# Performance work log

Hardware: AMD Instinct MI355X
Metric: run time of the kernel (lower is better)

## Reference

```python
import jax, jax.numpy as jnp
import numpy as np
from jax import lax

# fixed finite-difference kernels (HWIO)
KXN = jnp.asarray([[0., -1., 1.]], dtype=jnp.float32).reshape(1, 3, 1, 1)
KXP = jnp.asarray([[-1., 1., 0.]], dtype=jnp.float32).reshape(1, 3, 1, 1)
KYN = jnp.asarray([[1.], [-1.], [0.]], dtype=jnp.float32).reshape(3, 1, 1, 1)
KYP = jnp.asarray([[0.], [1.], [-1.]], dtype=jnp.float32).reshape(3, 1, 1, 1)


def conv2d(x, k):
    # NHWC input, HWIO kernel, SAME padding, stride 1
    return lax.conv_general_dilated(x, k, (1, 1), 'SAME',
                                    dimension_numbers=('NHWC', 'HWIO', 'NHWC'))


def setup_inputs() -> dict:
    key = jax.random.key(0)
    ks = jax.random.split(key, 11)
    B, H, W = 8, 512, 512
    return {
        'u': jax.random.normal(ks[0], (B, H, W, 1), jnp.float32),
        'image': jax.random.uniform(ks[1], (B, H, W, 1), jnp.float32),
        'conv_kernel_x': jax.random.normal(ks[2], (3, 3, 1, 32), jnp.float32) * 0.05,
        'conv_kernel_y': jax.random.normal(ks[3], (3, 3, 1, 32), jnp.float32) * 0.05,
        'sep_kernel_depthwise': jax.random.normal(ks[4], (3, 3, 1, 8), jnp.float32) * 0.05,
        'sep_kernel_pointwise': jax.random.normal(ks[5], (1, 1, 8, 8), jnp.float32) * 0.05,
        'conv_kernel_curve_0': jax.random.normal(ks[6], (5, 5, 1, 8), jnp.float32) * 0.05,
        'conv_kernel_curve_1': jax.random.normal(ks[7], (5, 5, 8, 8), jnp.float32) * 0.05,
        'conv_kernel_curve_2': jax.random.normal(ks[8], (3, 3, 8, 16), jnp.float32) * 0.05,
        'conv_kernel_smoother': jax.random.normal(ks[9], (5, 5, 1, 1), jnp.float32) * 0.05,
        'kappa_kernel': jax.random.normal(ks[10], (H, W, 1), jnp.float32) * 0.05,
    }


def reference(u, image, conv_kernel_x, conv_kernel_y, sep_kernel_depthwise,
              sep_kernel_pointwise, conv_kernel_curve_0, conv_kernel_curve_1,
              conv_kernel_curve_2, conv_kernel_smoother, kappa_kernel):
    # separable conv on the (fixed) image: in_ch=1 so depthwise == standard conv
    edges = conv2d(conv2d(image, sep_kernel_depthwise), sep_kernel_pointwise)
    edges = jnp.sum(jax.nn.relu(edges), axis=-1, keepdims=True)
    edges = jax.nn.soft_sign(edges)  # x / (1 + |x|)

    grad_edges_x = jnp.sum(jax.nn.relu(conv2d(edges, conv_kernel_x)), axis=-1, keepdims=True)
    grad_edges_y = jnp.sum(jax.nn.relu(conv2d(edges, conv_kernel_y)), axis=-1, keepdims=True)

    xp = conv2d(u, KXP)
    xn = conv2d(u, KXN)
    yp = conv2d(u, KYP)
    yn = conv2d(u, KYN)

    fxp = jax.nn.relu(grad_edges_x)
    fxn = -jax.nn.relu(-grad_edges_x)
    fyp = jax.nn.relu(grad_edges_y)
    fyn = -jax.nn.relu(-grad_edges_y)

    kappa = conv2d(conv2d(conv2d(u, conv_kernel_curve_0), conv_kernel_curve_1), conv_kernel_curve_2)
    kappa = jnp.sum(kappa, axis=-1, keepdims=True)
    kappa = kappa * kappa_kernel  # (H,W,1) broadcasts over batch
    kappa = conv2d(kappa, conv_kernel_smoother)

    return u + fxp * xp + fxn * xn + fyp * yp + fyn * yn + edges + kappa
```

## Files before the change

### kernel.cpp

```cpp
#include <hip/hip_runtime.h>
#include <cstddef>

#define HH 512
#define WW 512
#define BB 8
#define T  32

#define F0    256
#define KT0   1280
#define E0    4096
#define MAPW  520
#define MAPB  (512 * MAPW)
#define K0    (E0 + BB * MAPB)
#define WS_NEEDED_BYTES ((size_t)(K0 + BB * MAPB) * 4)

typedef __attribute__((ext_vector_type(8))) short short8;
typedef __attribute__((ext_vector_type(4))) float float4v;

__device__ inline unsigned short f2bf(float f) {
  unsigned u = __builtin_bit_cast(unsigned, f);
  unsigned r = (u + 0x7FFFu + ((u >> 16) & 1u)) >> 16;
  return (unsigned short)r;
}

__global__ __launch_bounds__(256) void precompute_kernels(
    const float* __restrict__ kd,
    const float* __restrict__ kp,
    const float* __restrict__ k0,
    const float* __restrict__ k1,
    const float* __restrict__ k2,
    const float* __restrict__ kx,
    const float* __restrict__ ky,
    float* __restrict__ ws) {
  __shared__ float k9[648];
  __shared__ float k2s[72];
  __shared__ float kef[121];
  const int tid = threadIdx.x;

  for (int idx = tid; idx < 72; idx += 256) {
    int c = idx & 7, pq = idx >> 3;
    float s = 0.f;
    for (int c0 = 0; c0 < 8; ++c0) s = fmaf(kd[pq * 8 + c0], kp[c0 * 8 + c], s);
    ws[idx] = s;
  }
  for (int idx = tid; idx < 72; idx += 256) {
    int c1 = idx & 7, tv = idx >> 3;
    float s = 0.f;
    for (int c2 = 0; c2 < 16; ++c2) s += k2[(tv * 8 + c1) * 16 + c2];
    k2s[idx] = s;
  }
  for (int idx = tid; idx < 648; idx += 256) {
    int c1 = idx & 7;
    int ab = idx >> 3;
    int a = ab / 9, b = ab % 9;
    float s = 0.f;
    int plo = a > 4 ? a - 4 : 0, phi = a < 4 ? a : 4;
    int qlo = b > 4 ? b - 4 : 0, qhi = b < 4 ? b : 4;
    for (int p = plo; p <= phi; ++p)
      for (int q = qlo; q <= qhi; ++q) {
        int r = a - p, sx = b - q;
        const float* k0p = &k0[(p * 5 + q) * 8];
        const float* k1p = &k1[((r * 5 + sx) * 8) * 8 + c1];
        for (int c0 = 0; c0 < 8; ++c0) s = fmaf(k0p[c0], k1p[c0 * 8], s);
      }
    k9[idx] = s;
  }
  for (int idx = tid; idx < 2048; idx += 256) {
    int nt = idx >> 9, ln = (idx >> 3) & 63, j = idx & 7;
    int k = (ln >> 4) * 8 + j;
    int n = nt * 16 + (ln & 15);
    float v = 0.f;
    if (k < 9) v = (n < 32) ? kx[k * 32 + n] : ky[k * 32 + (n - 32)];
    ((unsigned short*)ws)[F0 * 2 + idx] = f2bf(v);
  }
  __syncthreads();
  for (int idx = tid; idx < 121; idx += 256) {
    int A = idx / 11, B = idx % 11;
    float s = 0.f;
    int tlo = A > 8 ? A - 8 : 0, thi = A < 2 ? A : 2;
    int vlo = B > 8 ? B - 8 : 0, vhi = B < 2 ? B : 2;
    for (int t = tlo; t <= thi; ++t)
      for (int v = vlo; v <= vhi; ++v) {
        int a = A - t, b = B - v;
        for (int c1 = 0; c1 < 8; ++c1)
          s = fmaf(k9[(a * 9 + b) * 8 + c1], k2s[(t * 3 + v) * 8 + c1], s);
      }
    ws[72 + idx] = s;
    kef[idx] = s;
  }
  __syncthreads();
  for (int idx = tid; idx < 5632; idx += 256) {
    int b = idx >> 9, ln = (idx >> 3) & 63, j = idx & 7;
    int m = ln & 15;
    int k = (ln >> 4) * 8 + j;
    int a = k - m - 3;
    float v = ((unsigned)a < 11u) ? kef[a * 11 + b] : 0.f;
    ((unsigned short*)ws)[KT0 * 2 + idx] = f2bf(v);
  }
}

__global__ __launch_bounds__(256) void kernelA(
    const float* __restrict__ u, const float* __restrict__ img,
    const float* __restrict__ kk, const float* ws,
    float* maps) {
  __shared__ unsigned short suT[42 * 56];
  __shared__ float si[34 * 36];

  const int bx = blockIdx.x * T, by = blockIdx.y * T, b = blockIdx.z;
  const int tid = threadIdx.x;
  const float* ub = u + (size_t)b * HH * WW;
  const float* ib = img + (size_t)b * HH * WW;

  for (int idx = tid; idx < 48 * 42; idx += 256) {
    int r = idx / 42, c = idx % 42;
    int gy = by - 8 + r, gx = bx - 5 + c;
    float v = 0.f;
    if ((unsigned)gy < HH && (unsigned)gx < WW) v = ub[gy * WW + gx];
    suT[c * 56 + r] = f2bf(v);
  }
  for (int idx = tid; idx < 34 * 34; idx += 256) {
    int i = idx / 34, j = idx % 34;
    int gy = by - 1 + i, gx = bx - 1 + j;
    float v = 0.f;
    if ((unsigned)gy < HH && (unsigned)gx < WW) v = ib[gy * WW + gx];
    si[i * 36 + j] = v;
  }
  __syncthreads();

  {
    const int oy = tid >> 3, ox = (tid & 7) * 4;
    const int gy = by + oy, gx = bx + ox;

    float acc[8][4];
    #pragma unroll
    for (int c = 0; c < 8; ++c)
      #pragma unroll
      for (int t = 0; t < 4; ++t) acc[c][t] = 0.f;
    #pragma unroll
    for (int p = 0; p < 3; ++p) {
      const float* srow = &si[(oy + p) * 36 + ox];
      float4 r4 = *reinterpret_cast<const float4*>(srow);
      float2 r2 = *reinterpret_cast<const float2*>(srow + 4);
      float r[6] = {r4.x, r4.y, r4.z, r4.w, r2.x, r2.y};
      #pragma unroll
      for (int q = 0; q < 3; ++q) {
        float4 w0 = *reinterpret_cast<const float4*>(&ws[(p * 3 + q) * 8]);
        float4 w1 = *reinterpret_cast<const float4*>(&ws[(p * 3 + q) * 8 + 4]);
        #pragma unroll
        for (int t = 0; t < 4; ++t) {
          float v = r[q + t];
          acc[0][t] = fmaf(v, w0.x, acc[0][t]);
          acc[1][t] = fmaf(v, w0.y, acc[1][t]);
          acc[2][t] = fmaf(v, w0.z, acc[2][t]);
          acc[3][t] = fmaf(v, w0.w, acc[3][t]);
          acc[4][t] = fmaf(v, w1.x, acc[4][t]);
          acc[5][t] = fmaf(v, w1.y, acc[5][t]);
          acc[6][t] = fmaf(v, w1.z, acc[6][t]);
          acc[7][t] = fmaf(v, w1.w, acc[7][t]);
        }
      }
    }
    float ev[4];
    #pragma unroll
    for (int t = 0; t < 4; ++t) {
      float e = 0.f;
      #pragma unroll
      for (int c = 0; c < 8; ++c) e += fmaxf(acc[c][t], 0.f);
      ev[t] = e / (1.f + e);
    }
    float* erow = maps + E0 + (size_t)b * MAPB + (size_t)gy * MAPW + 4 + gx;
    *reinterpret_cast<float4*>(erow) = make_float4(ev[0], ev[1], ev[2], ev[3]);

    if (bx == 0 && (tid & 7) == 0) {
      float4 z = make_float4(0.f, 0.f, 0.f, 0.f);
      *reinterpret_cast<float4*>(maps + E0 + (size_t)b * MAPB + (size_t)gy * MAPW) = z;
      *reinterpret_cast<float4*>(maps + K0 + (size_t)b * MAPB + (size_t)gy * MAPW) = z;
    }
    if (bx == WW - T && (tid & 7) == 7) {
      float4 z = make_float4(0.f, 0.f, 0.f, 0.f);
      *reinterpret_cast<float4*>(maps + E0 + (size_t)b * MAPB + (size_t)gy * MAPW + 516) = z;
      *reinterpret_cast<float4*>(maps + K0 + (size_t)b * MAPB + (size_t)gy * MAPW + 516) = z;
    }
  }

  {
    const int lane = tid & 63;
    const int wv   = tid >> 6;
    const int q    = lane >> 4;
    const int n    = lane & 15;
    const int sty  = wv >> 1, stx = wv & 1;

    const unsigned short* KT = ((const unsigned short*)ws) + KT0 * 2;

    float4v acc = {0.f, 0.f, 0.f, 0.f};
    #pragma unroll
    for (int bb = 0; bb < 11; ++bb) {
      short8 af = *reinterpret_cast<const short8*>(KT + (bb * 64 + lane) * 8);
      short8 bf = *reinterpret_cast<const short8*>(
          &suT[(stx * 16 + n + bb) * 56 + sty * 16 + q * 8]);
      acc = __builtin_amdgcn_mfma_f32_16x16x32_bf16(af, bf, acc, 0, 0, 0);
    }
    float* kmapb = maps + K0 + (size_t)b * MAPB;
    #pragma unroll
    for (int i = 0; i < 4; ++i) {
      int yy = by + sty * 16 + q * 4 + i;
      int xx = bx + stx * 16 + n;
      kmapb[(size_t)yy * MAPW + 4 + xx] = acc[i] * kk[(size_t)yy * WW + xx];
    }
  }
}

__global__ __launch_bounds__(256) void kernelB(
    const float* __restrict__ u,
    const float* __restrict__ sm,
    const float* maps, float* __restrict__ out) {
  __shared__ float sgx[32 * 32];
  __shared__ float sgy[32 * 32];

  const int bx = blockIdx.x * T, by = blockIdx.y * T, b = blockIdx.z;
  const int tid = threadIdx.x;
  const float* emap = maps + E0 + (size_t)b * MAPB;
  const float* kmap = maps + K0 + (size_t)b * MAPB;
  const float* ub   = u + (size_t)b * HH * WW;

  const int lane = tid & 63;
  const int wv   = tid >> 6;
  const int q    = lane >> 4;
  const int m    = lane & 15;

  short8 afr[4];
  {
    const unsigned short* F = ((const unsigned short*)maps) + F0 * 2;
    #pragma unroll
    for (int t = 0; t < 4; ++t)
      afr[t] = *reinterpret_cast<const short8*>(F + (t * 64 + lane) * 8);
  }

  const int gy0 = by + wv * 8;

  #pragma unroll
  for (int h = 0; h < 32; h += 16) {
    const int gxl = bx + h + m;
    const float* colp = emap + 4 + gxl - 1;

    unsigned short W[9];
    #pragma unroll
    for (int d = 0; d < 3; ++d) {
      int ry = gy0 - 1 + d;
      int rc = ry < 0 ? 0 : (ry > HH - 1 ? HH - 1 : ry);
      float msk = (ry == rc) ? 1.f : 0.f;
      const float* rp = colp + (size_t)rc * MAPW;
      W[3 * d + 0] = f2bf(rp[0] * msk);
      W[3 * d + 1] = f2bf(rp[1] * msk);
      W[3 * d + 2] = f2bf(rp[2] * msk);
    }

    #pragma unroll
    for (int r = 0; r < 8; ++r) {
      short8 bv = (short8)0;
      if (q == 0) {
        #pragma unroll
        for (int j = 0; j < 8; ++j) bv[j] = (short)W[j];
      } else if (q == 1) {
        bv[0] = (short)W[8];
      }

      float4v c0 = {0.f, 0.f, 0.f, 0.f}, c1 = c0, c2 = c0, c3 = c0;
      c0 = __builtin_amdgcn_mfma_f32_16x16x32_bf16(afr[0], bv, c0, 0, 0, 0);
      c1 = __builtin_amdgcn_mfma_f32_16x16x32_bf16(afr[1], bv, c1, 0, 0, 0);
      c2 = __builtin_amdgcn_mfma_f32_16x16x32_bf16(afr[2], bv, c2, 0, 0, 0);
      c3 = __builtin_amdgcn_mfma_f32_16x16x32_bf16(afr[3], bv, c3, 0, 0, 0);

      float rx = 0.f, ry = 0.f;
      #pragma unroll
      for (int i = 0; i < 4; ++i) {
        rx += fmaxf(c0[i], 0.f) + fmaxf(c1[i], 0.f);
        ry += fmaxf(c2[i], 0.f) + fmaxf(c3[i], 0.f);
      }
      rx += __shfl_xor(rx, 16); rx += __shfl_xor(rx, 32);
      ry += __shfl_xor(ry, 16); ry += __shfl_xor(ry, 32);

      if (q == 0) {
        sgx[(wv * 8 + r) * 32 + h + m] = rx;
        sgy[(wv * 8 + r) * 32 + h + m] = ry;
      }

      if (r < 7) {
        #pragma unroll
        for (int t = 0; t < 6; ++t) W[t] = W[t + 3];
        int ryn = gy0 + r + 2;
        int rcn = ryn < 0 ? 0 : (ryn > HH - 1 ? HH - 1 : ryn);
        float msk = (ryn == rcn) ? 1.f : 0.f;
        const float* rp = colp + (size_t)rcn * MAPW;
        W[6] = f2bf(rp[0] * msk);
        W[7] = f2bf(rp[1] * msk);
        W[8] = f2bf(rp[2] * msk);
      }
    }
  }
  __syncthreads();

  {
    const int oy = tid >> 3, ox = (tid & 7) * 4;
    const int gy = by + oy, gx = bx + ox;

    float4 gx4 = *reinterpret_cast<const float4*>(&sgx[oy * 32 + ox]);
    float4 gy4 = *reinterpret_cast<const float4*>(&sgy[oy * 32 + ox]);
    float gxa[4] = {gx4.x, gx4.y, gx4.z, gx4.w};
    float gya[4] = {gy4.x, gy4.y, gy4.z, gy4.w};

    float4 ec4 = *reinterpret_cast<const float4*>(&emap[(size_t)gy * MAPW + 4 + gx]);
    float ec[4] = {ec4.x, ec4.y, ec4.z, ec4.w};

    float kap[4] = {0.f, 0.f, 0.f, 0.f};
    #pragma unroll
    for (int m5 = 0; m5 < 5; ++m5) {
      int ry = gy - 2 + m5;
      int rc = ry < 0 ? 0 : (ry > HH - 1 ? HH - 1 : ry);
      float msk = (ry == rc) ? 1.f : 0.f;
      const float* row = kmap + (size_t)rc * MAPW + 4 + gx;
      float2 a  = *reinterpret_cast<const float2*>(row - 2);
      float4 c4 = *reinterpret_cast<const float4*>(row);
      float2 d2 = *reinterpret_cast<const float2*>(row + 4);
      float r[8] = {a.x, a.y, c4.x, c4.y, c4.z, c4.w, d2.x, d2.y};
      #pragma unroll
      for (int n = 0; n < 5; ++n) {
        float w = sm[m5 * 5 + n] * msk;
        #pragma unroll
        for (int t = 0; t < 4; ++t) kap[t] = fmaf(r[t + n], w, kap[t]);
      }
    }

    const float* ur = ub + (size_t)gy * WW + gx;
    float4 uc4 = *reinterpret_cast<const float4*>(ur);
    int jm = gx > 0 ? -1 : 0;
    float ul = ur[jm];
    ul = gx > 0 ? ul : 0.f;
    int ryd = gy < HH - 1 ? gy + 1 : HH - 1;
    float md = gy < HH - 1 ? 1.f : 0.f;
    float4 ud4 = *reinterpret_cast<const float4*>(ub + (size_t)ryd * WW + gx);

    float uc[4]  = {uc4.x, uc4.y, uc4.z, uc4.w};
    float ulx[4] = {ul, uc4.x, uc4.y, uc4.z};
    float udn[4] = {ud4.x * md, ud4.y * md, ud4.z * md, ud4.w * md};

    float res[4];
    #pragma unroll
    for (int t = 0; t < 4; ++t) {
      float xp = uc[t] - ulx[t];
      float yp = uc[t] - udn[t];
      res[t] = uc[t] + gxa[t] * xp + gya[t] * yp + ec[t] + kap[t];
    }
    *reinterpret_cast<float4*>(&out[((size_t)b * HH + gy) * WW + gx]) =
        make_float4(res[0], res[1], res[2], res[3]);
  }
}

__global__ __launch_bounds__(256) void forcing_main(
    const float* __restrict__ u, const float* __restrict__ img,
    const float* __restrict__ kx, const float* __restrict__ ky,
    const float* __restrict__ sm, const float* __restrict__ kk,
    const float* __restrict__ ws, float* __restrict__ out) {
  __shared__ float su[46][48];
  __shared__ float si[36][37];
  __shared__ float se[34][35];
  __shared__ float sk[36][37];
  __shared__ float w_edge[72];
  __shared__ float w_kx[288];
  __shared__ float w_ky[288];
  __shared__ float w_k11[124];
  __shared__ float w_sm[28];

  const int bx = blockIdx.x * T;
  const int by = blockIdx.y * T;
  const int b  = blockIdx.z;
  const int tid = threadIdx.x;
  const float* ub = u   + (size_t)b * HH * WW;
  const float* ib = img + (size_t)b * HH * WW;

  for (int i = tid; i < 72; i += 256)  w_edge[i] = ws[i];
  for (int i = tid; i < 121; i += 256) w_k11[i]  = ws[72 + i];
  for (int i = tid; i < 288; i += 256) { w_kx[i] = kx[i]; w_ky[i] = ky[i]; }
  if (tid < 25) w_sm[tid] = sm[tid];

  for (int idx = tid; idx < 46 * 46; idx += 256) {
    int i = idx / 46, j = idx % 46;
    int gy = by - 7 + i, gx = bx - 7 + j;
    float v = 0.f;
    if ((unsigned)gy < HH && (unsigned)gx < WW) v = ub[gy * WW + gx];
    su[i][j] = v;
  }
  for (int idx = tid; idx < 36 * 36; idx += 256) {
    int i = idx / 36, j = idx % 36;
    int gy = by - 2 + i, gx = bx - 2 + j;
    float v = 0.f;
    if ((unsigned)gy < HH && (unsigned)gx < WW) v = ib[gy * WW + gx];
    si[i][j] = v;
  }
  __syncthreads();

  for (int idx = tid; idx < 34 * 9; idx += 256) {
    int i = idx / 9, j0 = (idx % 9) * 4;
    float acc[8][4];
    #pragma unroll
    for (int c = 0; c < 8; ++c)
      #pragma unroll
      for (int t = 0; t < 4; ++t) acc[c][t] = 0.f;
    #pragma unroll
    for (int p = 0; p < 3; ++p) {
      float r[6];
      #pragma unroll
      for (int t = 0; t < 6; ++t) r[t] = si[i + p][j0 + t];
      #pragma unroll
      for (int q = 0; q < 3; ++q) {
        const float4 w0 = *reinterpret_cast<const float4*>(&w_edge[(p * 3 + q) * 8]);
        const float4 w1 = *reinterpret_cast<const float4*>(&w_edge[(p * 3 + q) * 8 + 4]);
        #pragma unroll
        for (int t = 0; t < 4; ++t) {
          float v = r[q + t];
          acc[0][t] = fmaf(v, w0.x, acc[0][t]);
          acc[1][t] = fmaf(v, w0.y, acc[1][t]);
          acc[2][t] = fmaf(v, w0.z, acc[2][t]);
          acc[3][t] = fmaf(v, w0.w, acc[3][t]);
          acc[4][t] = fmaf(v, w1.x, acc[4][t]);
          acc[5][t] = fmaf(v, w1.y, acc[5][t]);
          acc[6][t] = fmaf(v, w1.z, acc[6][t]);
          acc[7][t] = fmaf(v, w1.w, acc[7][t]);
        }
      }
    }
    int gy = by - 1 + i;
    #pragma unroll
    for (int t = 0; t < 4; ++t) {
      int j = j0 + t;
      if (j < 34) {
        int gx = bx - 1 + j;
        float val = 0.f;
        if ((unsigned)gy < HH && (unsigned)gx < WW) {
          float e = 0.f;
          #pragma unroll
          for (int c = 0; c < 8; ++c) e += fmaxf(acc[c][t], 0.f);
          val = e / (1.f + e);
        }
        se[i][j] = val;
      }
    }
  }

  for (int idx = tid; idx < 36 * 9; idx += 256) {
    int i = idx / 9, js = (idx % 9) * 4;
    float o0 = 0.f, o1 = 0.f, o2 = 0.f, o3 = 0.f;
    #pragma unroll
    for (int A = 0; A < 11; ++A) {
      const float* row = &su[i + A][js];
      float4 v0 = *reinterpret_cast<const float4*>(row);
      float4 v1 = *reinterpret_cast<const float4*>(row + 4);
      float4 v2 = *reinterpret_cast<const float4*>(row + 8);
      float r[14] = {v0.x, v0.y, v0.z, v0.w, v1.x, v1.y, v1.z, v1.w,
                     v2.x, v2.y, v2.z, v2.w, row[12], row[13]};
      #pragma unroll
      for (int B2 = 0; B2 < 11; ++B2) {
        float w = w_k11[A * 11 + B2];
        o0 = fmaf(r[B2],     w, o0);
        o1 = fmaf(r[B2 + 1], w, o1);
        o2 = fmaf(r[B2 + 2], w, o2);
        o3 = fmaf(r[B2 + 3], w, o3);
      }
    }
    int gy = by - 2 + i;
    float o[4] = {o0, o1, o2, o3};
    #pragma unroll
    for (int t = 0; t < 4; ++t) {
      int gx = bx - 2 + js + t;
      float val = 0.f;
      if ((unsigned)gy < HH && (unsigned)gx < WW) val = o[t] * kk[gy * WW + gx];
      sk[i][js + t] = val;
    }
  }
  __syncthreads();

  {
    const int oy = tid >> 3;
    const int ox = (tid & 7) * 4;
    const int gy = by + oy;
    const int gx = bx + ox;

    float e[3][6];
    #pragma unroll
    for (int p = 0; p < 3; ++p)
      #pragma unroll
      for (int t = 0; t < 6; ++t) e[p][t] = se[oy + p][ox + t];

    const float4* wx4 = reinterpret_cast<const float4*>(w_kx);
    const float4* wy4 = reinterpret_cast<const float4*>(w_ky);

    float gxa[4] = {0.f, 0.f, 0.f, 0.f};
    float gya[4] = {0.f, 0.f, 0.f, 0.f};
    #pragma unroll
    for (int cq = 0; cq < 8; ++cq) {
      float sx[4][4], sy[4][4];
      #pragma unroll
      for (int cc = 0; cc < 4; ++cc)
        #pragma unroll
        for (int t = 0; t < 4; ++t) { sx[cc][t] = 0.f; sy[cc][t] = 0.f; }
      #pragma unroll
      for (int p = 0; p < 3; ++p)
        #pragma unroll
        for (int q = 0; q < 3; ++q) {
          float4 wx = wx4[(p * 3 + q) * 8 + cq];
          float4 wy = wy4[(p * 3 + q) * 8 + cq];
          #pragma unroll
          for (int t = 0; t < 4; ++t) {
            float evv = e[p][q + t];
            sx[0][t] = fmaf(evv, wx.x, sx[0][t]);
            sx[1][t] = fmaf(evv, wx.y, sx[1][t]);
            sx[2][t] = fmaf(evv, wx.z, sx[2][t]);
            sx[3][t] = fmaf(evv, wx.w, sx[3][t]);
            sy[0][t] = fmaf(evv, wy.x, sy[0][t]);
            sy[1][t] = fmaf(evv, wy.y, sy[1][t]);
            sy[2][t] = fmaf(evv, wy.z, sy[2][t]);
            sy[3][t] = fmaf(evv, wy.w, sy[3][t]);
          }
        }
      #pragma unroll
      for (int cc = 0; cc < 4; ++cc)
        #pragma unroll
        for (int t = 0; t < 4; ++t) {
          gxa[t] += fmaxf(sx[cc][t], 0.f);
          gya[t] += fmaxf(sy[cc][t], 0.f);
        }
    }

    float res[4];
    #pragma unroll
    for (int t = 0; t < 4; ++t) {
      float kap = 0.f;
      #pragma unroll
      for (int m = 0; m < 5; ++m)
        #pragma unroll
        for (int n = 0; n < 5; ++n)
          kap = fmaf(sk[oy + m][ox + t + n], w_sm[m * 5 + n], kap);

      float uc = su[oy + 7][ox + 7 + t];
      float xp = uc - su[oy + 7][ox + 6 + t];
      float yp = uc - su[oy + 8][ox + 7 + t];
      float ec = se[oy + 1][ox + 1 + t];
      res[t] = uc + gxa[t] * xp + gya[t] * yp + ec + kap;
    }

    float4 r4 = make_float4(res[0], res[1], res[2], res[3]);
    *reinterpret_cast<float4*>(&out[((size_t)b * HH + gy) * WW + gx]) = r4;
  }
}

extern "C" void kernel_launch(void* const* d_in, const int* in_sizes, int n_in,
                              void* d_out, int out_size, void* d_ws, size_t ws_size,
                              hipStream_t stream) {
  const float* u   = (const float*)d_in[0];
  const float* img = (const float*)d_in[1];
  const float* kx  = (const float*)d_in[2];
  const float* ky  = (const float*)d_in[3];
  const float* kd  = (const float*)d_in[4];
  const float* kp  = (const float*)d_in[5];
  const float* k0  = (const float*)d_in[6];
  const float* k1  = (const float*)d_in[7];
  const float* k2  = (const float*)d_in[8];
  const float* sm  = (const float*)d_in[9];
  const float* kk  = (const float*)d_in[10];
  float* out = (float*)d_out;
  float* ws  = (float*)d_ws;

  precompute_kernels<<<1, 256, 0, stream>>>(kd, kp, k0, k1, k2, kx, ky, ws);
  dim3 grid(WW / T, HH / T, BB);
  if (ws != nullptr && ws_size >= WS_NEEDED_BYTES) {
    kernelA<<<grid, 256, 0, stream>>>(u, img, kk, ws, ws);
    kernelB<<<grid, 256, 0, stream>>>(u, sm, ws, out);
  } else {
    forcing_main<<<grid, 256, 0, stream>>>(u, img, kx, ky, sm, kk, ws, out);
  }
}
```

Before: 143.8 us.

## Fuse edge/kappa map kernel and gradient/output kernel into one halo-recompute kernel

Merges the two-pass pipeline (kernelA writing edge and kappa maps to global workspace, kernelB reading them back) into a single kernel that keeps those intermediate maps in shared memory. Each tile now computes edges and kappa over an enlarged halo (34x34 and 36x36) so the neighbouring 3x3 and 5x5 stencils can be applied locally. This removes the global write/read of two 8x512x520 float maps and one kernel launch. In exchange it adds redundant halo computation, more MFMA tiles (9 instead of 4) and much larger LDS use, which may lower occupancy.

```diff
diff --git a/kernel.cpp b/kernel.cpp
--- a/kernel.cpp
+++ b/kernel.cpp
@@ -8,11 +8,7 @@
 
 #define F0    256
 #define KT0   1280
-#define E0    4096
-#define MAPW  520
-#define MAPB  (512 * MAPW)
-#define K0    (E0 + BB * MAPB)
-#define WS_NEEDED_BYTES ((size_t)(K0 + BB * MAPB) * 4)
+#define WS_NEEDED_BYTES ((size_t)4096 * 4)
 
 typedef __attribute__((ext_vector_type(8))) short short8;
 typedef __attribute__((ext_vector_type(4))) float float4v;
@@ -99,38 +95,46 @@
   }
 }
 
-__global__ __launch_bounds__(256) void kernelA(
+__global__ __launch_bounds__(256) void fused(
     const float* __restrict__ u, const float* __restrict__ img,
-    const float* __restrict__ kk, const float* ws,
-    float* maps) {
-  __shared__ unsigned short suT[42 * 56];
-  __shared__ float si[34 * 36];
+    const float* __restrict__ kk, const float* __restrict__ sm,
+    const float* __restrict__ ws, float* __restrict__ out) {
+  __shared__ unsigned short suT[58 * 72];
+  __shared__ float si[36 * 36];
+  __shared__ float se32[34 * 35];
+  __shared__ unsigned short sebf[34 * 36];
+  __shared__ float skp[36 * 37];
+  __shared__ float sgx[32 * 32];
+  __shared__ float sgy[32 * 32];
 
   const int bx = blockIdx.x * T, by = blockIdx.y * T, b = blockIdx.z;
   const int tid = threadIdx.x;
   const float* ub = u + (size_t)b * HH * WW;
   const float* ib = img + (size_t)b * HH * WW;
 
-  for (int idx = tid; idx < 48 * 42; idx += 256) {
-    int r = idx / 42, c = idx % 42;
-    int gy = by - 8 + r, gx = bx - 5 + c;
+  const int lane = tid & 63;
+  const int wv   = tid >> 6;
+  const int q    = lane >> 4;
+  const int m    = lane & 15;
+
+  for (int idx = tid; idx < 64 * 58; idx += 256) {
+    int r = idx / 58, c = idx % 58;
+    int gy = by - 10 + r, gx = bx - 7 + c;
     float v = 0.f;
     if ((unsigned)gy < HH && (unsigned)gx < WW) v = ub[gy * WW + gx];
-    suT[c * 56 + r] = f2bf(v);
-  }
-  for (int idx = tid; idx < 34 * 34; idx += 256) {
-    int i = idx / 34, j = idx % 34;
-    int gy = by - 1 + i, gx = bx - 1 + j;
+    suT[c * 72 + r] = f2bf(v);
+  }
+  for (int idx = tid; idx < 36 * 36; idx += 256) {
+    int i = idx / 36, j = idx % 36;
+    int gy = by - 2 + i, gx = bx - 2 + j;
     float v = 0.f;
     if ((unsigned)gy < HH && (unsigned)gx < WW) v = ib[gy * WW + gx];
     si[i * 36 + j] = v;
   }
   __syncthreads();
 
-  {
-    const int oy = tid >> 3, ox = (tid & 7) * 4;
-    const int gy = by + oy, gx = bx + ox;
-
+  for (int idx = tid; idx < 34 * 9; idx += 256) {
+    int i = idx / 9, j0 = (idx % 9) * 4;
     float acc[8][4];
     #pragma unroll
     for (int c = 0; c < 8; ++c)
@@ -138,17 +142,16 @@
       for (int t = 0; t < 4; ++t) acc[c][t] = 0.f;
     #pragma unroll
     for (int p = 0; p < 3; ++p) {
-      const float* srow = &si[(oy + p) * 36 + ox];
-      float4 r4 = *reinterpret_cast<const float4*>(srow);
-      float2 r2 = *reinterpret_cast<const float2*>(srow + 4);
-      float r[6] = {r4.x, r4.y, r4.z, r4.w, r2.x, r2.y};
-      #pragma unroll
-      for (int q = 0; q < 3; ++q) {
-        float4 w0 = *reinterpret_cast<const float4*>(&ws[(p * 3 + q) * 8]);
-        float4 w1 = *reinterpret_cast<const float4*>(&ws[(p * 3 + q) * 8 + 4]);
+      float r[6];
+      #pragma unroll
+      for (int t = 0; t < 6; ++t) r[t] = si[(i + p) * 36 + j0 + t];
+      #pragma unroll
+      for (int qq = 0; qq < 3; ++qq) {
+        float4 w0 = *reinterpret_cast<const float4*>(&ws[(p * 3 + qq) * 8]);
+        float4 w1 = *reinterpret_cast<const float4*>(&ws[(p * 3 + qq) * 8 + 4]);
         #pragma unroll
         for (int t = 0; t < 4; ++t) {
-          float v = r[q + t];
+          float v = r[qq + t];
           acc[0][t] = fmaf(v, w0.x, acc[0][t]);
           acc[1][t] = fmaf(v, w0.y, acc[1][t]);
           acc[2][t] = fmaf(v, w0.z, acc[2][t]);
@@ -160,141 +163,105 @@
         }
       }
     }
-    float ev[4];
+    int gy = by - 1 + i;
     #pragma unroll
     for (int t = 0; t < 4; ++t) {
-      float e = 0.f;
-      #pragma unroll
-      for (int c = 0; c < 8; ++c) e += fmaxf(acc[c][t], 0.f);
-      ev[t] = e / (1.f + e);
-    }
-    float* erow = maps + E0 + (size_t)b * MAPB + (size_t)gy * MAPW + 4 + gx;
-    *reinterpret_cast<float4*>(erow) = make_float4(ev[0], ev[1], ev[2], ev[3]);
-
-    if (bx == 0 && (tid & 7) == 0) {
-      float4 z = make_float4(0.f, 0.f, 0.f, 0.f);
-      *reinterpret_cast<float4*>(maps + E0 + (size_t)b * MAPB + (size_t)gy * MAPW) = z;
-      *reinterpret_cast<float4*>(maps + K0 + (size_t)b * MAPB + (size_t)gy * MAPW) = z;
-    }
-    if (bx == WW - T && (tid & 7) == 7) {
-      float4 z = make_float4(0.f, 0.f, 0.f, 0.f);
-      *reinterpret_cast<float4*>(maps + E0 + (size_t)b * MAPB + (size_t)gy * MAPW + 516) = z;
-      *reinterpret_cast<float4*>(maps + K0 + (size_t)b * MAPB + (size_t)gy * MAPW + 516) = z;
+      int j = j0 + t;
+      if (j < 34) {
+        int gx = bx - 1 + j;
+        float val = 0.f;
+        if ((unsigned)gy < HH && (unsigned)gx < WW) {
+          float e = 0.f;
+          #pragma unroll
+          for (int c = 0; c < 8; ++c) e += fmaxf(acc[c][t], 0.f);
+          val = e / (1.f + e);
+        }
+        se32[i * 35 + j] = val;
+        sebf[i * 36 + j] = f2bf(val);
+      }
     }
   }
 
   {
-    const int lane = tid & 63;
-    const int wv   = tid >> 6;
-    const int q    = lane >> 4;
-    const int n    = lane & 15;
-    const int sty  = wv >> 1, stx = wv & 1;
-
     const unsigned short* KT = ((const unsigned short*)ws) + KT0 * 2;
-
-    float4v acc = {0.f, 0.f, 0.f, 0.f};
-    #pragma unroll
-    for (int bb = 0; bb < 11; ++bb) {
-      short8 af = *reinterpret_cast<const short8*>(KT + (bb * 64 + lane) * 8);
-      short8 bf = *reinterpret_cast<const short8*>(
-          &suT[(stx * 16 + n + bb) * 56 + sty * 16 + q * 8]);
-      acc = __builtin_amdgcn_mfma_f32_16x16x32_bf16(af, bf, acc, 0, 0, 0);
-    }
-    float* kmapb = maps + K0 + (size_t)b * MAPB;
-    #pragma unroll
-    for (int i = 0; i < 4; ++i) {
-      int yy = by + sty * 16 + q * 4 + i;
-      int xx = bx + stx * 16 + n;
-      kmapb[(size_t)yy * MAPW + 4 + xx] = acc[i] * kk[(size_t)yy * WW + xx];
-    }
-  }
-}
-
-__global__ __launch_bounds__(256) void kernelB(
-    const float* __restrict__ u,
-    const float* __restrict__ sm,
-    const float* maps, float* __restrict__ out) {
-  __shared__ float sgx[32 * 32];
-  __shared__ float sgy[32 * 32];
-
-  const int bx = blockIdx.x * T, by = blockIdx.y * T, b = blockIdx.z;
-  const int tid = threadIdx.x;
-  const float* emap = maps + E0 + (size_t)b * MAPB;
-  const float* kmap = maps + K0 + (size_t)b * MAPB;
-  const float* ub   = u + (size_t)b * HH * WW;
-
-  const int lane = tid & 63;
-  const int wv   = tid >> 6;
-  const int q    = lane >> 4;
-  const int m    = lane & 15;
-
-  short8 afr[4];
+    for (int s = wv; s < 9; s += 4) {
+      int sty = s / 3, stx = s % 3;
+      float4v acc = {0.f, 0.f, 0.f, 0.f};
+      #pragma unroll
+      for (int bb = 0; bb < 11; ++bb) {
+        short8 af = *reinterpret_cast<const short8*>(KT + (bb * 64 + lane) * 8);
+        short8 bf = *reinterpret_cast<const short8*>(
+            &suT[(stx * 16 + m + bb) * 72 + sty * 16 + q * 8]);
+        acc = __builtin_amdgcn_mfma_f32_16x16x32_bf16(af, bf, acc, 0, 0, 0);
+      }
+      #pragma unroll
+      for (int i = 0; i < 4; ++i) {
+        int rl = sty * 16 + q * 4 + i, cl = stx * 16 + m;
+        if (rl < 36 && cl < 36) {
+          int yy = by - 2 + rl, xx = bx - 2 + cl;
+          float v = 0.f;
+          if ((unsigned)yy < HH && (unsigned)xx < WW)
+            v = acc[i] * kk[(size_t)yy * WW + xx];
+          skp[rl * 37 + cl] = v;
+        }
+      }
+    }
+  }
+  __syncthreads();
+
   {
-    const unsigned short* F = ((const unsigned short*)maps) + F0 * 2;
+    short8 afr[4];
+    const unsigned short* F = ((const unsigned short*)ws) + F0 * 2;
     #pragma unroll
     for (int t = 0; t < 4; ++t)
       afr[t] = *reinterpret_cast<const short8*>(F + (t * 64 + lane) * 8);
-  }
-
-  const int gy0 = by + wv * 8;
-
-  #pragma unroll
-  for (int h = 0; h < 32; h += 16) {
-    const int gxl = bx + h + m;
-    const float* colp = emap + 4 + gxl - 1;
-
-    unsigned short W[9];
-    #pragma unroll
-    for (int d = 0; d < 3; ++d) {
-      int ry = gy0 - 1 + d;
-      int rc = ry < 0 ? 0 : (ry > HH - 1 ? HH - 1 : ry);
-      float msk = (ry == rc) ? 1.f : 0.f;
-      const float* rp = colp + (size_t)rc * MAPW;
-      W[3 * d + 0] = f2bf(rp[0] * msk);
-      W[3 * d + 1] = f2bf(rp[1] * msk);
-      W[3 * d + 2] = f2bf(rp[2] * msk);
-    }
-
-    #pragma unroll
-    for (int r = 0; r < 8; ++r) {
-      short8 bv = (short8)0;
-      if (q == 0) {
-        #pragma unroll
-        for (int j = 0; j < 8; ++j) bv[j] = (short)W[j];
-      } else if (q == 1) {
-        bv[0] = (short)W[8];
-      }
-
-      float4v c0 = {0.f, 0.f, 0.f, 0.f}, c1 = c0, c2 = c0, c3 = c0;
-      c0 = __builtin_amdgcn_mfma_f32_16x16x32_bf16(afr[0], bv, c0, 0, 0, 0);
-      c1 = __builtin_amdgcn_mfma_f32_16x16x32_bf16(afr[1], bv, c1, 0, 0, 0);
-      c2 = __builtin_amdgcn_mfma_f32_16x16x32_bf16(afr[2], bv, c2, 0, 0, 0);
-      c3 = __builtin_amdgcn_mfma_f32_16x16x32_bf16(afr[3], bv, c3, 0, 0, 0);
-
-      float rx = 0.f, ry = 0.f;
-      #pragma unroll
-      for (int i = 0; i < 4; ++i) {
-        rx += fmaxf(c0[i], 0.f) + fmaxf(c1[i], 0.f);
-        ry += fmaxf(c2[i], 0.f) + fmaxf(c3[i], 0.f);
-      }
-      rx += __shfl_xor(rx, 16); rx += __shfl_xor(rx, 32);
-      ry += __shfl_xor(ry, 16); ry += __shfl_xor(ry, 32);
-
-      if (q == 0) {
-        sgx[(wv * 8 + r) * 32 + h + m] = rx;
-        sgy[(wv * 8 + r) * 32 + h + m] = ry;
-      }
-
-      if (r < 7) {
-        #pragma unroll
-        for (int t = 0; t < 6; ++t) W[t] = W[t + 3];
-        int ryn = gy0 + r + 2;
-        int rcn = ryn < 0 ? 0 : (ryn > HH - 1 ? HH - 1 : ryn);
-        float msk = (ryn == rcn) ? 1.f : 0.f;
-        const float* rp = colp + (size_t)rcn * MAPW;
-        W[6] = f2bf(rp[0] * msk);
-        W[7] = f2bf(rp[1] * msk);
-        W[8] = f2bf(rp[2] * msk);
+
+    #pragma unroll
+    for (int h = 0; h < 32; h += 16) {
+      const int cl = h + m;
+      unsigned short W[9];
+      #pragma unroll
+      for (int d = 0; d < 3; ++d) {
+        const unsigned short* rp = &sebf[(wv * 8 + d) * 36 + cl];
+        W[3 * d + 0] = rp[0]; W[3 * d + 1] = rp[1]; W[3 * d + 2] = rp[2];
+      }
+
+      #pragma unroll
+      for (int r = 0; r < 8; ++r) {
+        short8 bv = (short8)0;
+        if (q == 0) {
+          #pragma unroll
+          for (int j = 0; j < 8; ++j) bv[j] = (short)W[j];
+        } else if (q == 1) {
+          bv[0] = (short)W[8];
+        }
+
+        float4v c0 = {0.f, 0.f, 0.f, 0.f}, c1 = c0, c2 = c0, c3 = c0;
+        c0 = __builtin_amdgcn_mfma_f32_16x16x32_bf16(afr[0], bv, c0, 0, 0, 0);
+        c1 = __builtin_amdgcn_mfma_f32_16x16x32_bf16(afr[1], bv, c1, 0, 0, 0);
+        c2 = __builtin_amdgcn_mfma_f32_16x16x32_bf16(afr[2], bv, c2, 0, 0, 0);
+        c3 = __builtin_amdgcn_mfma_f32_16x16x32_bf16(afr[3], bv, c3, 0, 0, 0);
+
+        float rx = 0.f, ry = 0.f;
+        #pragma unroll
+        for (int i = 0; i < 4; ++i) {
+          rx += fmaxf(c0[i], 0.f) + fmaxf(c1[i], 0.f);
+          ry += fmaxf(c2[i], 0.f) + fmaxf(c3[i], 0.f);
+        }
+        rx += __shfl_xor(rx, 16); rx += __shfl_xor(rx, 32);
+        ry += __shfl_xor(ry, 16); ry += __shfl_xor(ry, 32);
+
+        if (q == 0) {
+          sgx[(wv * 8 + r) * 32 + cl] = rx;
+          sgy[(wv * 8 + r) * 32 + cl] = ry;
+        }
+
+        if (r < 7) {
+          #pragma unroll
+          for (int t = 0; t < 6; ++t) W[t] = W[t + 3];
+          const unsigned short* rp = &sebf[(wv * 8 + r + 3) * 36 + cl];
+          W[6] = rp[0]; W[7] = rp[1]; W[8] = rp[2];
+        }
       }
     }
   }
@@ -309,23 +276,16 @@
     float gxa[4] = {gx4.x, gx4.y, gx4.z, gx4.w};
     float gya[4] = {gy4.x, gy4.y, gy4.z, gy4.w};
 
-    float4 ec4 = *reinterpret_cast<const float4*>(&emap[(size_t)gy * MAPW + 4 + gx]);
-    float ec[4] = {ec4.x, ec4.y, ec4.z, ec4.w};
-
     float kap[4] = {0.f, 0.f, 0.f, 0.f};
     #pragma unroll
     for (int m5 = 0; m5 < 5; ++m5) {
-      int ry = gy - 2 + m5;
-      int rc = ry < 0 ? 0 : (ry > HH - 1 ? HH - 1 : ry);
-      float msk = (ry == rc) ? 1.f : 0.f;
-      const float* row = kmap + (size_t)rc * MAPW + 4 + gx;
-      float2 a  = *reinterpret_cast<const float2*>(row - 2);
-      float4 c4 = *reinterpret_cast<const float4*>(row);
-      float2 d2 = *reinterpret_cast<const float2*>(row + 4);
-      float r[8] = {a.x, a.y, c4.x, c4.y, c4.z, c4.w, d2.x, d2.y};
+      const float* row = &skp[(oy + m5) * 37 + ox];
+      float r[8];
+      #pragma unroll
+      for (int t = 0; t < 8; ++t) r[t] = row[t];
       #pragma unroll
       for (int n = 0; n < 5; ++n) {
-        float w = sm[m5 * 5 + n] * msk;
+        float w = sm[m5 * 5 + n];
         #pragma unroll
         for (int t = 0; t < 4; ++t) kap[t] = fmaf(r[t + n], w, kap[t]);
       }
@@ -349,7 +309,8 @@
     for (int t = 0; t < 4; ++t) {
       float xp = uc[t] - ulx[t];
       float yp = uc[t] - udn[t];
-      res[t] = uc[t] + gxa[t] * xp + gya[t] * yp + ec[t] + kap[t];
+      float ec = se32[(oy + 1) * 35 + ox + 1 + t];
+      res[t] = uc[t] + gxa[t] * xp + gya[t] * yp + ec + kap[t];
     }
     *reinterpret_cast<float4*>(&out[((size_t)b * HH + gy) * WW + gx]) =
         make_float4(res[0], res[1], res[2], res[3]);
@@ -573,8 +534,7 @@
   precompute_kernels<<<1, 256, 0, stream>>>(kd, kp, k0, k1, k2, kx, ky, ws);
   dim3 grid(WW / T, HH / T, BB);
   if (ws != nullptr && ws_size >= WS_NEEDED_BYTES) {
-    kernelA<<<grid, 256, 0, stream>>>(u, img, kk, ws, ws);
-    kernelB<<<grid, 256, 0, stream>>>(u, sm, ws, out);
+    fused<<<grid, 256, 0, stream>>>(u, img, kk, sm, ws, out);
   } else {
     forcing_main<<<grid, 256, 0, stream>>>(u, img, kx, ky, sm, kk, ws, out);
   }
```

New measurement: 146.8 us. +2.1%, slower.
